# Kernel tuning notes

Hardware: AMD Instinct MI355X
Metric: run time of the kernel (lower is better)

Reference implementation:

```python
import jax, jax.numpy as jnp
import numpy as np

B, N, C, K = 4, 4096, 64, 16
EPS = 1e-5


def _bn(x, g, b, m, v):
    # eval-mode BatchNorm2d on [B, C, N, K]
    scale = (g / jnp.sqrt(v + EPS))[None, :, None, None]
    return (x - m[None, :, None, None]) * scale + b[None, :, None, None]


def setup_inputs() -> dict:
    key = jax.random.key(0)
    ks = jax.random.split(key, 32)
    s = 0.05
    inp = {
        "p": jax.random.normal(ks[0], (B, N, 3), jnp.float32),
        "x": jax.random.normal(ks[1], (B, C, N), jnp.float32),
        "mask": jnp.ones((B, N), dtype=bool),
        # q/k/v 1x1 Conv1d weights [out, in] + bias
        "Wq": jax.random.normal(ks[2], (C, C)) * s, "bq": jax.random.normal(ks[3], (C,)) * s,
        "Wk": jax.random.normal(ks[4], (C, C)) * s, "bk": jax.random.normal(ks[5], (C,)) * s,
        "Wv": jax.random.normal(ks[6], (C, C)) * s, "bv": jax.random.normal(ks[7], (C,)) * s,
        # pos-enc: Conv2d(3->C, no bias), BN, ReLU, Conv2d(C->C)
        "pe_w1": jax.random.normal(ks[8], (C, 3)) * s,
        "pe_bn_g": jax.random.normal(ks[9], (C,)) * s + 1.0,
        "pe_bn_b": jax.random.normal(ks[10], (C,)) * s,
        "pe_bn_m": jax.random.normal(ks[11], (C,)) * s,
        "pe_bn_v": jax.random.uniform(ks[12], (C,), minval=0.5, maxval=1.5),
        "pe_w2": jax.random.normal(ks[13], (C, C)) * s, "pe_b2": jax.random.normal(ks[14], (C,)) * s,
        # attn: BN, ReLU, Conv2d(C->C, no bias), BN, ReLU, Conv2d(C->C)
        "at_bn0_g": jax.random.normal(ks[15], (C,)) * s + 1.0,
        "at_bn0_b": jax.random.normal(ks[16], (C,)) * s,
        "at_bn0_m": jax.random.normal(ks[17], (C,)) * s,
        "at_bn0_v": jax.random.uniform(ks[18], (C,), minval=0.5, maxval=1.5),
        "at_w1": jax.random.normal(ks[19], (C, C)) * s,
        "at_bn1_g": jax.random.normal(ks[20], (C,)) * s + 1.0,
        "at_bn1_b": jax.random.normal(ks[21], (C,)) * s,
        "at_bn1_m": jax.random.normal(ks[22], (C,)) * s,
        "at_bn1_v": jax.random.uniform(ks[23], (C,), minval=0.5, maxval=1.5),
        "at_w2": jax.random.normal(ks[24], (C, C)) * s, "at_b2": jax.random.normal(ks[25], (C,)) * s,
    }
    return inp


def reference(p, x, mask, Wq, bq, Wk, bk, Wv, bv,
              pe_w1, pe_bn_g, pe_bn_b, pe_bn_m, pe_bn_v, pe_w2, pe_b2,
              at_bn0_g, at_bn0_b, at_bn0_m, at_bn0_v, at_w1,
              at_bn1_g, at_bn1_b, at_bn1_m, at_bn1_v, at_w2, at_b2):
    # q, k, v: 1x1 Conv1d -> [B, C, N]
    q = jnp.einsum('oc,bcn->bon', Wq, x) + bq[None, :, None]
    k = jnp.einsum('oc,bcn->bon', Wk, x) + bk[None, :, None]
    v = jnp.einsum('oc,bcn->bon', Wv, x) + bv[None, :, None]

    # ---- knn_point(K, p, p): Euclidean cdist, zero-point masking, topk smallest
    sq = jnp.sum(p * p, axis=-1)                                   # [B, N]
    d2 = sq[:, :, None] + sq[:, None, :] - 2.0 * jnp.einsum('bnc,bmc->bnm', p, p)
    dist = jnp.sqrt(jnp.maximum(d2, 0.0))                          # [B, N, N]
    valid = ~jnp.all(p == 0, axis=-1)                              # [B, N]
    dist = jnp.where(valid[:, None, :], dist, jnp.inf)
    _, idx = jax.lax.top_k(-dist, K)                               # [B, N, K]

    gather = jax.vmap(lambda a, i: a[i])                           # ([N,C],[N,K]) -> [N,K,C]
    n_k = gather(jnp.transpose(k, (0, 2, 1)), idx)                 # [B, N, K, C]
    n_v = gather(jnp.transpose(v, (0, 2, 1)), idx)                 # [B, N, K, C]
    n_p = gather(p, idx)                                           # [B, N, K, 3]

    rel = p[:, :, None, :] - n_p                                   # [B, N, K, 3]
    rel = jnp.transpose(rel, (0, 3, 1, 2))                         # [B, 3, N, K]

    # position encoding MLP
    h = jnp.einsum('oc,bcnk->bonk', pe_w1, rel)
    h = jax.nn.relu(_bn(h, pe_bn_g, pe_bn_b, pe_bn_m, pe_bn_v))
    n_r = jnp.einsum('oc,bcnk->bonk', pe_w2, h) + pe_b2[None, :, None, None]  # [B,C,N,K]

    # attention MLP on (q - n_k + n_r)
    a = q[:, :, :, None] - jnp.transpose(n_k, (0, 3, 1, 2)) + n_r
    a = jax.nn.relu(_bn(a, at_bn0_g, at_bn0_b, at_bn0_m, at_bn0_v))
    a = jnp.einsum('oc,bcnk->bonk', at_w1, a)
    a = jax.nn.relu(_bn(a, at_bn1_g, at_bn1_b, at_bn1_m, at_bn1_v))
    a = jnp.einsum('oc,bcnk->bonk', at_w2, a) + at_b2[None, :, None, None]

    # mask [B,N] broadcast to [B,C,N,K] (masks query rows, as in original)
    a = jnp.where(mask[:, None, :, None], a, -1e10)
    a = jax.nn.softmax(a, axis=-1)
    a = jnp.where(jnp.isnan(a), 0.0, a)

    y = jnp.sum(a * (jnp.transpose(n_v, (0, 3, 1, 2)) + n_r), axis=-1)  # [B, C, N]
    return (p, y)
```

## Files before the change

### kernel.cpp

```cpp
#include <hip/hip_runtime.h>
#include <stdint.h>

#define NB 4
#define NP 4096
#define NC 64
#define NK 16
#define BN_EPS 1e-5f

typedef __attribute__((ext_vector_type(8))) short short8;
typedef __attribute__((ext_vector_type(4))) float f32x4;
typedef unsigned long long u64;

__device__ __forceinline__ short f2bf(float f) {
    unsigned u = __float_as_uint(f);
    unsigned r = (u + 0x7FFFu + ((u >> 16) & 1u)) >> 16;
    return (short)(unsigned short)r;
}

__global__ __launch_bounds__(256) void px_kernel(const float* __restrict__ p,
                                                 float4* __restrict__ px,
                                                 float* __restrict__ pcopy) {
    int gid = blockIdx.x * 256 + threadIdx.x;
    float x = p[gid * 3 + 0], y = p[gid * 3 + 1], z = p[gid * 3 + 2];
    pcopy[gid * 3 + 0] = x; pcopy[gid * 3 + 1] = y; pcopy[gid * 3 + 2] = z;
    float sq = fmaf(z, z, fmaf(y, y, x * x));
    bool inv = (x == 0.0f) && (y == 0.0f) && (z == 0.0f);
    px[gid] = make_float4(x, y, z, inv ? __builtin_inff() : sq);
}

#define KQW 2
#define KNB 2048
#define KCAP 64

__global__ __launch_bounds__(256) void prep_kernel(
        const float4* __restrict__ px, int* __restrict__ idxout,
        const float* __restrict__ x,
        const float* __restrict__ Wq, const float* __restrict__ bq,
        const float* __restrict__ Wk, const float* __restrict__ bk,
        const float* __restrict__ Wv, const float* __restrict__ bv,
        float* __restrict__ outbase) {
    __shared__ __align__(16) char smem[NC * NC * 4 + NC * 4];

    if (blockIdx.x < KNB) {
        u64 (*sbuf)[KCAP] = (u64 (*)[KCAP])smem;
        float (*tb)[KQW * 64] = (float (*)[KQW * 64])(smem + 4096);
        int* scnt = (int*)(smem + 4096 + 2048);

        const int l = threadIdx.x & 63;
        const int w = threadIdx.x >> 6;
        const int gw = blockIdx.x * 4 + w;
        const int q0 = gw * KQW;
        const int b  = q0 >> 12;
        const float4* pb = px + (size_t)b * NP;

        float4 pn[KQW];
#pragma unroll
        for (int j = 0; j < KQW; ++j) pn[j] = px[q0 + j];
        if (l < KQW) scnt[w * KQW + l] = 0;
        __builtin_amdgcn_wave_barrier();

        float k1[KQW];
#pragma unroll
        for (int j = 0; j < KQW; ++j) k1[j] = __builtin_inff();
#pragma unroll 4
        for (int i = 0; i < NP / 64; ++i) {
            float4 pm = pb[i * 64 + l];
#pragma unroll
            for (int j = 0; j < KQW; ++j) {
                float dot = fmaf(pm.z, pn[j].z, fmaf(pm.y, pn[j].y, pm.x * pn[j].x));
                float d2  = fmaf(-2.0f, dot, pn[j].w + pm.w);
                k1[j] = fminf(k1[j], d2);
            }
        }
#pragma unroll
        for (int j = 0; j < KQW; ++j) tb[w][j * 64 + l] = k1[j];
        __builtin_amdgcn_wave_barrier();

        float T[KQW];
#pragma unroll
        for (int j = 0; j < KQW; ++j) {
            const float* tj = &tb[w][j * 64];
            int rank = 0;
#pragma unroll 4
            for (int t = 0; t < 64; t += 4) {
                f32x4 v = *(const f32x4*)&tj[t];
                rank += (v[0] < k1[j]) + (v[1] < k1[j]) + (v[2] < k1[j]) + (v[3] < k1[j]);
            }
            float cand = (rank <= 15) ? k1[j] : -__builtin_inff();
#pragma unroll
            for (int off = 32; off; off >>= 1)
                cand = fmaxf(cand, __shfl_xor(cand, off));
            T[j] = cand;
        }

#pragma unroll 2
        for (int i = 0; i < NP / 64; ++i) {
            int m = i * 64 + l;
            float4 pm = pb[m];
#pragma unroll
            for (int j = 0; j < KQW; ++j) {
                float dot = fmaf(pm.z, pn[j].z, fmaf(pm.y, pn[j].y, pm.x * pn[j].x));
                float d2  = fmaf(-2.0f, dot, pn[j].w + pm.w);
                if (d2 <= T[j]) {
                    int pos = atomicAdd(&scnt[w * KQW + j], 1);
                    if (pos < KCAP) {
                        float d2c = fmaxf(d2, 0.0f);
                        sbuf[w * KQW + j][pos] =
                            ((u64)__float_as_uint(d2c) << 32) | (unsigned int)m;
                    }
                }
            }
        }
        __builtin_amdgcn_wave_barrier();

#pragma unroll 1
        for (int j = 0; j < KQW; ++j) {
            int cnt = scnt[w * KQW + j];
            if (cnt > KCAP) cnt = KCAP;
            if (l < cnt) {
                const u64* sb = sbuf[w * KQW + j];
                u64 kj = sb[l];
                int rank = 0;
                for (int t = 0; t < cnt; ++t) rank += (sb[t] < kj);
                if (rank < NK)
                    idxout[(size_t)(q0 + j) * NK + rank] = (int)(kj & 0xffffffffu);
            }
        }
    } else {
        float* wt  = (float*)smem;
        float* bsh = (float*)(smem + NC * NC * 4);

        const int qb    = blockIdx.x - KNB;
        const int which = qb >> 8;
        const int bxl   = qb & 255;
        const float* W    = which == 0 ? Wq : which == 1 ? Wk : Wv;
        const float* bias = which == 0 ? bq : which == 1 ? bk : bv;
        float* out = outbase + (size_t)which * NB * NP * NC;

        for (int e = threadIdx.x; e < NC * NC; e += 256)
            wt[(e & 63) * NC + (e >> 6)] = W[e];
        if (threadIdx.x < NC) bsh[threadIdx.x] = bias[threadIdx.x];
        __syncthreads();

        const int gid   = bxl * 256 + threadIdx.x;
        const int token = gid & (NB * NP - 1);
        const int qtr   = gid >> 14;
        const int b = token >> 12, n = token & (NP - 1);

        float acc[16];
#pragma unroll
        for (int o = 0; o < 16; ++o) acc[o] = bsh[qtr * 16 + o];

        const float* xp = x + (size_t)b * NC * NP + n;
#pragma unroll 4
        for (int c = 0; c < NC; ++c) {
            float xc = xp[(size_t)c * NP];
            const float4* wr = (const float4*)&wt[c * NC + qtr * 16];
#pragma unroll
            for (int o4 = 0; o4 < 4; ++o4) {
                float4 w4 = wr[o4];
                acc[o4 * 4 + 0] = fmaf(w4.x, xc, acc[o4 * 4 + 0]);
                acc[o4 * 4 + 1] = fmaf(w4.y, xc, acc[o4 * 4 + 1]);
                acc[o4 * 4 + 2] = fmaf(w4.z, xc, acc[o4 * 4 + 2]);
                acc[o4 * 4 + 3] = fmaf(w4.w, xc, acc[o4 * 4 + 3]);
            }
        }
        float4* op = (float4*)(out + (size_t)token * NC + qtr * 16);
#pragma unroll
        for (int o4 = 0; o4 < 4; ++o4)
            op[o4] = make_float4(acc[o4 * 4 + 0], acc[o4 * 4 + 1],
                                 acc[o4 * 4 + 2], acc[o4 * 4 + 3]);
    }
}

#define QPW 4
#define HBSTR 72

__device__ __forceinline__ short8 pack8(float4 a, float4 b) {
    short8 r;
    r[0] = f2bf(a.x); r[1] = f2bf(a.y); r[2] = f2bf(a.z); r[3] = f2bf(a.w);
    r[4] = f2bf(b.x); r[5] = f2bf(b.y); r[6] = f2bf(b.z); r[7] = f2bf(b.w);
    return r;
}

__device__ __forceinline__ void gemm_stage_lds(const short8 (*__restrict__ WFm)[64],
                                               int l,
                                               const unsigned short* HBw,
                                               float* DBw, int tok, int quad) {
    short8 b0 = *(const short8*)((const char*)HBw + tok * (HBSTR * 2) + quad * 16);
    short8 b1 = *(const short8*)((const char*)HBw + tok * (HBSTR * 2) + 64 + quad * 16);
#pragma unroll
    for (int ob = 0; ob < 4; ++ob) {
        f32x4 acc = {0.0f, 0.0f, 0.0f, 0.0f};
        short8 a0 = WFm[ob * 2 + 0][l];
        short8 a1 = WFm[ob * 2 + 1][l];
        acc = __builtin_amdgcn_mfma_f32_16x16x32_bf16(a0, b0, acc, 0, 0, 0);
        acc = __builtin_amdgcn_mfma_f32_16x16x32_bf16(a1, b1, acc, 0, 0, 0);
#pragma unroll
        for (int r = 0; r < 4; ++r) {
            int row = ob * 16 + quad * 4 + r;
            DBw[tok * 64 + (row ^ tok)] = acc[r];
        }
    }
}

__global__ __launch_bounds__(256, 4) void fused_mfma_kernel(
        const float4* __restrict__ px, const int* __restrict__ idx,
        const float* __restrict__ qT, const float* __restrict__ kT,
        const float* __restrict__ vT,
        const float* __restrict__ pe_w1,
        const float* __restrict__ pe_g, const float* __restrict__ pe_b,
        const float* __restrict__ pe_m, const float* __restrict__ pe_v,
        const float* __restrict__ pe_w2, const float* __restrict__ pe_b2,
        const float* __restrict__ b0g, const float* __restrict__ b0b,
        const float* __restrict__ b0m, const float* __restrict__ b0v,
        const float* __restrict__ at_w1,
        const float* __restrict__ b1g, const float* __restrict__ b1b,
        const float* __restrict__ b1m, const float* __restrict__ b1v,
        const float* __restrict__ at_w2, const float* __restrict__ at_b2,
        float* __restrict__ yout) {
    __shared__ __align__(16) short8 WFl[3][8][64];
    __shared__ __align__(16) float UB[4][16 * 64];

    const int l    = threadIdx.x & 63;
    const int w    = threadIdx.x >> 6;
    const int c    = l;
    const int tok  = l & 15;
    const int quad = l >> 4;

    if (w < 3) {
        const float* Wm = w == 0 ? pe_w2 : w == 1 ? at_w1 : at_w2;
#pragma unroll
        for (int ob = 0; ob < 4; ++ob)
#pragma unroll
            for (int ch = 0; ch < 2; ++ch) {
                const float* src = Wm + (ob * 16 + tok) * NC + ch * 32 + quad * 8;
                float4 a = *(const float4*)src;
                float4 bq4 = *(const float4*)(src + 4);
                WFl[w][ob * 2 + ch][l] = pack8(a, bq4);
            }
    }

    const float pw0 = pe_w1[c * 3 + 0], pw1 = pe_w1[c * 3 + 1], pw2v = pe_w1[c * 3 + 2];
    const float pes = pe_g[c] / sqrtf(pe_v[c] + BN_EPS);
    const float peb = fmaf(-pe_m[c], pes, pe_b[c]);
    const float s0  = b0g[c] / sqrtf(b0v[c] + BN_EPS);
    const float bb0 = fmaf(-b0m[c], s0, b0b[c]);
    const float s1  = b1g[c] / sqrtf(b1v[c] + BN_EPS);
    const float bb1 = fmaf(-b1m[c], s1, b1b[c]);
    const float peb2 = pe_b2[c];
    const float ab2  = at_b2[c];

    __syncthreads();

    unsigned short* HBw = (unsigned short*)UB[w];
    float* DBw = UB[w];

    const int batch = blockIdx.x & 3;
    const int gwb   = (blockIdx.x >> 2) * 4 + w;
    const int q0s   = batch * NP + gwb * QPW;

    for (int jq = 0; jq < QPW; ++jq) {
        const int qi = q0s + jq;
        const int b = qi >> 12, n = qi & (NP - 1);
        const int bNP = b * NP;
        const float4 pn = px[qi];
        const float qv = qT[(size_t)qi * NC + c];

        const int4* ip = (const int4*)(idx + (size_t)qi * NK);
        int4 nid0 = ip[0], nid1 = ip[1], nid2 = ip[2], nid3 = ip[3];
        int mreg[NK];
        mreg[0]  = __builtin_amdgcn_readfirstlane(nid0.x);
        mreg[1]  = __builtin_amdgcn_readfirstlane(nid0.y);
        mreg[2]  = __builtin_amdgcn_readfirstlane(nid0.z);
        mreg[3]  = __builtin_amdgcn_readfirstlane(nid0.w);
        mreg[4]  = __builtin_amdgcn_readfirstlane(nid1.x);
        mreg[5]  = __builtin_amdgcn_readfirstlane(nid1.y);
        mreg[6]  = __builtin_amdgcn_readfirstlane(nid1.z);
        mreg[7]  = __builtin_amdgcn_readfirstlane(nid1.w);
        mreg[8]  = __builtin_amdgcn_readfirstlane(nid2.x);
        mreg[9]  = __builtin_amdgcn_readfirstlane(nid2.y);
        mreg[10] = __builtin_amdgcn_readfirstlane(nid2.z);
        mreg[11] = __builtin_amdgcn_readfirstlane(nid2.w);
        mreg[12] = __builtin_amdgcn_readfirstlane(nid3.x);
        mreg[13] = __builtin_amdgcn_readfirstlane(nid3.y);
        mreg[14] = __builtin_amdgcn_readfirstlane(nid3.z);
        mreg[15] = __builtin_amdgcn_readfirstlane(nid3.w);

        const float4* pxb = px + (size_t)bNP;

#pragma unroll
        for (int h8 = 0; h8 < 2; ++h8) {
            float4 pmr[8];
#pragma unroll
            for (int k = 0; k < 8; ++k) pmr[k] = pxb[mreg[h8 * 8 + k]];
#pragma unroll
            for (int k = 0; k < 8; ++k) {
                float r0 = pn.x - pmr[k].x, r1 = pn.y - pmr[k].y, r2 = pn.z - pmr[k].z;
                float h = fmaf(pw2v, r2, fmaf(pw1, r1, pw0 * r0));
                h = fmaxf(fmaf(h, pes, peb), 0.0f);
                HBw[(h8 * 8 + k) * HBSTR + c] = (unsigned short)f2bf(h);
            }
        }
        __builtin_amdgcn_wave_barrier();

        gemm_stage_lds(WFl[0], l, HBw, DBw, tok, quad);
        __builtin_amdgcn_wave_barrier();

        float nr[NK];
#pragma unroll
        for (int t = 0; t < NK; ++t)
            nr[t] = DBw[t * 64 + (c ^ t)] + peb2;
        __builtin_amdgcn_wave_barrier();

#pragma unroll
        for (int h8 = 0; h8 < 2; ++h8) {
            float kv[8];
#pragma unroll
            for (int k = 0; k < 8; ++k)
                kv[k] = kT[((size_t)(bNP + mreg[h8 * 8 + k])) * NC + c];
#pragma unroll
            for (int k = 0; k < 8; ++k) {
                const int t = h8 * 8 + k;
                float a0 = qv - kv[k] + nr[t];
                a0 = fmaxf(fmaf(a0, s0, bb0), 0.0f);
                HBw[t * HBSTR + c] = (unsigned short)f2bf(a0);
            }
        }
        __builtin_amdgcn_wave_barrier();

        gemm_stage_lds(WFl[1], l, HBw, DBw, tok, quad);
        __builtin_amdgcn_wave_barrier();

        float a1r[NK];
#pragma unroll
        for (int t = 0; t < NK; ++t)
            a1r[t] = DBw[t * 64 + (c ^ t)];
        __builtin_amdgcn_wave_barrier();
#pragma unroll
        for (int t = 0; t < NK; ++t) {
            float a2 = fmaxf(fmaf(a1r[t], s1, bb1), 0.0f);
            HBw[t * HBSTR + c] = (unsigned short)f2bf(a2);
        }
        __builtin_amdgcn_wave_barrier();

        gemm_stage_lds(WFl[2], l, HBw, DBw, tok, quad);
        __builtin_amdgcn_wave_barrier();

        float mxr = -__builtin_inff();
#pragma unroll
        for (int t = 0; t < NK; ++t)
            mxr = fmaxf(mxr, DBw[t * 64 + (c ^ t)]);
        const float mx = mxr + ab2;
        float ssum = 0.0f, yacc = 0.0f;
#pragma unroll
        for (int h8 = 0; h8 < 2; ++h8) {
            float vv[8];
#pragma unroll
            for (int k = 0; k < 8; ++k)
                vv[k] = vT[((size_t)(bNP + mreg[h8 * 8 + k])) * NC + c];
#pragma unroll
            for (int k = 0; k < 8; ++k) {
                const int t = h8 * 8 + k;
                float e = __expf((DBw[t * 64 + (c ^ t)] + ab2) - mx);
                ssum += e;
                yacc = fmaf(e, vv[k] + nr[t], yacc);
            }
        }
        yout[((size_t)(b * NC + c)) * NP + n] = yacc / ssum;
        __builtin_amdgcn_wave_barrier();
    }
}

extern "C" void kernel_launch(void* const* d_in, const int* in_sizes, int n_in,
                              void* d_out, int out_size, void* d_ws, size_t ws_size,
                              hipStream_t stream) {
    const float* p    = (const float*)d_in[0];
    const float* x    = (const float*)d_in[1];
    const float* Wq = (const float*)d_in[3];  const float* bq = (const float*)d_in[4];
    const float* Wk = (const float*)d_in[5];  const float* bk = (const float*)d_in[6];
    const float* Wv = (const float*)d_in[7];  const float* bv = (const float*)d_in[8];
    const float* pe_w1 = (const float*)d_in[9];
    const float* pe_g  = (const float*)d_in[10]; const float* pe_b = (const float*)d_in[11];
    const float* pe_m  = (const float*)d_in[12]; const float* pe_v = (const float*)d_in[13];
    const float* pe_w2 = (const float*)d_in[14]; const float* pe_b2 = (const float*)d_in[15];
    const float* b0g = (const float*)d_in[16]; const float* b0b = (const float*)d_in[17];
    const float* b0m = (const float*)d_in[18]; const float* b0v = (const float*)d_in[19];
    const float* at_w1 = (const float*)d_in[20];
    const float* b1g = (const float*)d_in[21]; const float* b1b = (const float*)d_in[22];
    const float* b1m = (const float*)d_in[23]; const float* b1v = (const float*)d_in[24];
    const float* at_w2 = (const float*)d_in[25]; const float* at_b2 = (const float*)d_in[26];

    const size_t BNC = (size_t)NB * NP * NC;
    float* ws  = (float*)d_ws;
    float* qT  = ws;
    float* kT  = qT + BNC;
    float* vT  = kT + BNC;
    float4* px = (float4*)(vT + BNC);
    int* idx   = (int*)(px + (size_t)NB * NP);

    float* outp = (float*)d_out;
    float* y = outp + (size_t)NB * NP * 3;

    px_kernel<<<dim3(64), dim3(256), 0, stream>>>(p, px, outp);
    prep_kernel<<<dim3(KNB + 768), dim3(256), 0, stream>>>(
        px, idx, x, Wq, bq, Wk, bk, Wv, bv, qT);
    fused_mfma_kernel<<<dim3(1024), dim3(256), 0, stream>>>(
        px, idx, qT, kT, vT, pe_w1, pe_g, pe_b, pe_m, pe_v, pe_w2, pe_b2,
        b0g, b0b, b0m, b0v, at_w1, b1g, b1b, b1m, b1v, at_w2, at_b2, y);
}
```

Baseline: 202.6 us.

## Split kNN candidate scan across four waves per query group

Each kNN block now handles 4 queries, and the 4 waves split the 4096-point scan into quarters instead of one wave scanning every point for 2 queries. Per-lane minima are combined across waves through shared memory to pick the threshold, and the filtered candidates from all waves are gathered into shared per-query buffers before a rank sort done by one wave per query. The QKV projection blocks now come first in the grid. This shortens the serial scan per wave and raises parallelism, at the cost of block-wide syncs and shared-memory atomics across waves.

```diff
diff --git a/kernel.cpp b/kernel.cpp
--- a/kernel.cpp
+++ b/kernel.cpp
@@ -28,9 +28,9 @@
     px[gid] = make_float4(x, y, z, inv ? __builtin_inff() : sq);
 }
 
-#define KQW 2
-#define KNB 2048
 #define KCAP 64
+#define NQKV 768
+#define KNB  4096
 
 __global__ __launch_bounds__(256) void prep_kernel(
         const float4* __restrict__ px, int* __restrict__ idxout,
@@ -41,52 +41,66 @@
         float* __restrict__ outbase) {
     __shared__ __align__(16) char smem[NC * NC * 4 + NC * 4];
 
-    if (blockIdx.x < KNB) {
+    if (blockIdx.x >= NQKV) {
         u64 (*sbuf)[KCAP] = (u64 (*)[KCAP])smem;
-        float (*tb)[KQW * 64] = (float (*)[KQW * 64])(smem + 4096);
-        int* scnt = (int*)(smem + 4096 + 2048);
-
-        const int l = threadIdx.x & 63;
-        const int w = threadIdx.x >> 6;
-        const int gw = blockIdx.x * 4 + w;
-        const int q0 = gw * KQW;
+        float (*tb)[256]  = (float (*)[256])(smem + 2048);
+        float* tbc        = (float*)(smem + 2048 + 4096);
+        int* scnt         = (int*)(smem + 2048 + 4096 + 1024);
+
+        const int l  = threadIdx.x & 63;
+        const int w  = threadIdx.x >> 6;
+        const int kb = blockIdx.x - NQKV;
+        const int q0 = kb * 4;
         const int b  = q0 >> 12;
         const float4* pb = px + (size_t)b * NP;
 
-        float4 pn[KQW];
-#pragma unroll
-        for (int j = 0; j < KQW; ++j) pn[j] = px[q0 + j];
-        if (l < KQW) scnt[w * KQW + l] = 0;
-        __builtin_amdgcn_wave_barrier();
-
-        float k1[KQW];
-#pragma unroll
-        for (int j = 0; j < KQW; ++j) k1[j] = __builtin_inff();
+        float4 pn[4];
+#pragma unroll
+        for (int j = 0; j < 4; ++j) pn[j] = px[q0 + j];
+        if (threadIdx.x < 4) scnt[threadIdx.x] = 0;
+
+        const int i0 = w * 16;
+        float k1[4];
+#pragma unroll
+        for (int j = 0; j < 4; ++j) k1[j] = __builtin_inff();
 #pragma unroll 4
-        for (int i = 0; i < NP / 64; ++i) {
-            float4 pm = pb[i * 64 + l];
-#pragma unroll
-            for (int j = 0; j < KQW; ++j) {
+        for (int i = 0; i < 16; ++i) {
+            float4 pm = pb[(i0 + i) * 64 + l];
+#pragma unroll
+            for (int j = 0; j < 4; ++j) {
                 float dot = fmaf(pm.z, pn[j].z, fmaf(pm.y, pn[j].y, pm.x * pn[j].x));
                 float d2  = fmaf(-2.0f, dot, pn[j].w + pm.w);
                 k1[j] = fminf(k1[j], d2);
             }
         }
 #pragma unroll
-        for (int j = 0; j < KQW; ++j) tb[w][j * 64 + l] = k1[j];
-        __builtin_amdgcn_wave_barrier();
-
-        float T[KQW];
-#pragma unroll
-        for (int j = 0; j < KQW; ++j) {
-            const float* tj = &tb[w][j * 64];
+        for (int j = 0; j < 4; ++j) tb[w][j * 64 + l] = k1[j];
+        __syncthreads();
+
+        float k1c[4];
+#pragma unroll
+        for (int j = 0; j < 4; ++j) {
+            float m0 = fminf(tb[0][j * 64 + l], tb[1][j * 64 + l]);
+            float m1 = fminf(tb[2][j * 64 + l], tb[3][j * 64 + l]);
+            k1c[j] = fminf(m0, m1);
+        }
+        if (w == 0) {
+#pragma unroll
+            for (int j = 0; j < 4; ++j) tbc[j * 64 + l] = k1c[j];
+        }
+        __syncthreads();
+
+        float T[4];
+#pragma unroll
+        for (int j = 0; j < 4; ++j) {
+            const float* tj = &tbc[j * 64];
             int rank = 0;
 #pragma unroll 4
             for (int t = 0; t < 64; t += 4) {
                 f32x4 v = *(const f32x4*)&tj[t];
-                rank += (v[0] < k1[j]) + (v[1] < k1[j]) + (v[2] < k1[j]) + (v[3] < k1[j]);
-            }
-            float cand = (rank <= 15) ? k1[j] : -__builtin_inff();
+                rank += (v[0] < k1c[j]) + (v[1] < k1c[j]) + (v[2] < k1c[j]) + (v[3] < k1c[j]);
+            }
+            float cand = (rank <= 15) ? k1c[j] : -__builtin_inff();
 #pragma unroll
             for (int off = 32; off; off >>= 1)
                 cand = fmaxf(cand, __shfl_xor(cand, off));
@@ -94,43 +108,42 @@
         }
 
 #pragma unroll 2
-        for (int i = 0; i < NP / 64; ++i) {
-            int m = i * 64 + l;
+        for (int i = 0; i < 16; ++i) {
+            int m = (i0 + i) * 64 + l;
             float4 pm = pb[m];
 #pragma unroll
-            for (int j = 0; j < KQW; ++j) {
+            for (int j = 0; j < 4; ++j) {
                 float dot = fmaf(pm.z, pn[j].z, fmaf(pm.y, pn[j].y, pm.x * pn[j].x));
                 float d2  = fmaf(-2.0f, dot, pn[j].w + pm.w);
                 if (d2 <= T[j]) {
-                    int pos = atomicAdd(&scnt[w * KQW + j], 1);
+                    int pos = atomicAdd(&scnt[j], 1);
                     if (pos < KCAP) {
                         float d2c = fmaxf(d2, 0.0f);
-                        sbuf[w * KQW + j][pos] =
-                            ((u64)__float_as_uint(d2c) << 32) | (unsigned int)m;
+                        sbuf[j][pos] = ((u64)__float_as_uint(d2c) << 32)
+                                       | (unsigned int)m;
                     }
                 }
             }
         }
-        __builtin_amdgcn_wave_barrier();
-
-#pragma unroll 1
-        for (int j = 0; j < KQW; ++j) {
-            int cnt = scnt[w * KQW + j];
+        __syncthreads();
+
+        {
+            int cnt = scnt[w];
             if (cnt > KCAP) cnt = KCAP;
             if (l < cnt) {
-                const u64* sb = sbuf[w * KQW + j];
+                const u64* sb = sbuf[w];
                 u64 kj = sb[l];
                 int rank = 0;
                 for (int t = 0; t < cnt; ++t) rank += (sb[t] < kj);
                 if (rank < NK)
-                    idxout[(size_t)(q0 + j) * NK + rank] = (int)(kj & 0xffffffffu);
+                    idxout[(size_t)(q0 + w) * NK + rank] = (int)(kj & 0xffffffffu);
             }
         }
     } else {
         float* wt  = (float*)smem;
         float* bsh = (float*)(smem + NC * NC * 4);
 
-        const int qb    = blockIdx.x - KNB;
+        const int qb    = blockIdx.x;
         const int which = qb >> 8;
         const int bxl   = qb & 255;
         const float* W    = which == 0 ? Wq : which == 1 ? Wk : Wv;
@@ -403,7 +416,7 @@
     float* y = outp + (size_t)NB * NP * 3;
 
     px_kernel<<<dim3(64), dim3(256), 0, stream>>>(p, px, outp);
-    prep_kernel<<<dim3(KNB + 768), dim3(256), 0, stream>>>(
+    prep_kernel<<<dim3(NQKV + KNB), dim3(256), 0, stream>>>(
         px, idx, x, Wq, bq, Wk, bk, Wv, bv, qT);
     fused_mfma_kernel<<<dim3(1024), dim3(256), 0, stream>>>(
         px, idx, qT, kT, vT, pe_w1, pe_g, pe_b, pe_m, pe_v, pe_w2, pe_b2,
```

After: 205.7 us. No clear change (+1.5%).
